# Performance work log

Hardware: AMD Instinct MI355X
Metric: run time of the kernel (lower is better)

The kernel has to match this reference:

```python
import jax, jax.numpy as jnp
import numpy as np

B, S, N, D = 2, 2048, 16, 64


def setup_inputs() -> dict:
    key = jax.random.key(0)
    kq, kk, kv = jax.random.split(key, 3)
    query = jax.random.normal(kq, (B, S, N, D), dtype=jnp.float32)
    key_t = jax.random.normal(kk, (B, S, N, D), dtype=jnp.float32)
    value = jax.random.normal(kv, (B, S, N, D), dtype=jnp.float32)
    mask = jnp.ones((B, 1, S, S), dtype=jnp.int32)
    return {"query": query, "key": key_t, "value": value, "mask": mask}


def reference(query, key, value, mask):
    d_k = query.shape[-1]
    # [b, n, q, k] attention scores
    scores = jnp.einsum('bqnd,bknd->bnqk', query, key) / jnp.sqrt(jnp.float32(d_k))
    scores = jnp.where(mask == 0, -jnp.inf, scores)
    # NOTE: faithful to the source, softmax is over dim=1 (the HEAD axis),
    # not the key axis. Dropout prob is 0.0 -> identity.
    attn_weights = jax.nn.softmax(scores, axis=1)
    out = jnp.einsum('bnqk,bknd->bnqd', attn_weights, value)
    return out
```

## Files before the change

### kernel.cpp

```cpp
#include <hip/hip_runtime.h>
#include <hip/hip_bf16.h>


#define B_ 2
#define S_ 2048
#define N_ 16
#define D_ 64
#define TQ 32
#define TK 32
#define NT 64

typedef __bf16 bf16x4 __attribute__((ext_vector_type(4)));
typedef __bf16 bf16x8 __attribute__((ext_vector_type(8)));
typedef float  f32x16 __attribute__((ext_vector_type(16)));
typedef unsigned int uint32x4 __attribute__((ext_vector_type(4)));

#define QSCALE 0.18033688011112042f

static __device__ __forceinline__ unsigned int cvt_pk_bf16(float a, float b) {
    unsigned int r;
    asm("v_cvt_pk_bf16_f32 %0, %1, %2" : "=v"(r) : "v"(a), "v"(b));
    return r;
}
static __device__ __forceinline__ void permlane_swap(unsigned int& a, unsigned int& b) {
    asm("v_permlane32_swap_b32 %0, %1" : "+v"(a), "+v"(b));
}

__global__ __launch_bounds__(256) void cvt_qk_pack_kernel(
    const float* __restrict__ Qf, const float* __restrict__ Kf,
    __bf16* __restrict__ QP, __bf16* __restrict__ KP)
{
    const int z = blockIdx.z;
    const float* src = (z < B_) ? Qf : Kf;
    __bf16*      dst = (z < B_) ? QP : KP;
    const float scale = (z < B_) ? QSCALE : 1.0f;
    const int b  = (z < B_) ? z : z - B_;
    const int n  = blockIdx.y;
    const int st = blockIdx.x;
    const int t  = threadIdx.x;
    const int ks   = t >> 6;
    const int lane = t & 63;
    const int lo   = lane & 31;
    const int hi   = lane >> 5;

    const float* p = &src[(((size_t)b * S_ + st * 32 + lo) * N_ + n) * D_ + ks * 16 + hi * 8];
    const float4 a0 = *(const float4*)p;
    const float4 a1 = *(const float4*)(p + 4);
    bf16x8 o;
    o[0] = (__bf16)(a0.x * scale); o[1] = (__bf16)(a0.y * scale);
    o[2] = (__bf16)(a0.z * scale); o[3] = (__bf16)(a0.w * scale);
    o[4] = (__bf16)(a1.x * scale); o[5] = (__bf16)(a1.y * scale);
    o[6] = (__bf16)(a1.z * scale); o[7] = (__bf16)(a1.w * scale);
    *(bf16x8*)&dst[(((size_t)b * N_ + n) * NT + st) * 2048 + (size_t)t * 8] = o;
}

__global__ __launch_bounds__(256) void cvt_v_pack_kernel(
    const float* __restrict__ V, __bf16* __restrict__ VP)
{
    __shared__ __bf16 tile[64][68];
    const int s0 = blockIdx.x * 64;
    const int n  = blockIdx.y;
    const int b  = blockIdx.z;
    const int t  = threadIdx.x;

    {
        const int d4 = (t & 15) * 4;
        const int sr = t >> 4;
        #pragma unroll
        for (int r = 0; r < 4; ++r) {
            const int s = sr + r * 16;
            const float4 v = *(const float4*)&V[(((size_t)b * S_ + s0 + s) * N_ + n) * D_ + d4];
            tile[s][d4 + 0] = (__bf16)v.x;
            tile[s][d4 + 1] = (__bf16)v.y;
            tile[s][d4 + 2] = (__bf16)v.z;
            tile[s][d4 + 3] = (__bf16)v.w;
        }
    }
    __syncthreads();
    {
        const int kstep = t >> 7;
        const int dt    = (t >> 6) & 1;
        const int lane  = t & 63;
        const int lo    = lane & 31;
        const int hi    = lane >> 5;
        #pragma unroll
        for (int kt_sub = 0; kt_sub < 2; ++kt_sub) {
            bf16x8 o;
            #pragma unroll
            for (int j = 0; j < 8; ++j)
                o[j] = tile[kt_sub * 32 + kstep * 16 + hi * 8 + j][dt * 32 + lo];
            const size_t kt = (size_t)(blockIdx.x * 2 + kt_sub);
            *(bf16x8*)&VP[(((size_t)b * N_ + n) * NT + kt) * 2048 + (size_t)t * 8] = o;
        }
    }
}

__global__ __launch_bounds__(256, 2) void pass1_z_kernel(
    const __bf16* __restrict__ QP, const __bf16* __restrict__ KP,
    const int* __restrict__ M, float* __restrict__ Zr)
{
    const int tid  = threadIdx.x;
    const int wv   = tid >> 6;
    const int lane = tid & 63;
    const int lo   = lane & 31;
    const int hi   = lane >> 5;

    const int ktA = (blockIdx.x * 4 + wv) * 2;
    const int qt0 = blockIdx.y * 2;
    const int b   = blockIdx.z;
    const int k0A = ktA * TK;
    const int q0  = qt0 * TQ;

    const __bf16* Qp = QP + ((size_t)b * N_ * NT + qt0) * 2048 + (size_t)lane * 8;
    const __bf16* Kp = KP + ((size_t)b * N_ * NT + ktA) * 2048 + (size_t)lane * 8;

    f32x16 zAA = {}, zAB = {}, zBA = {}, zBB = {};
    for (int h = 0; h < N_; ++h) {
        const __bf16* Qh = Qp + (size_t)h * NT * 2048;
        const __bf16* Kh = Kp + (size_t)h * NT * 2048;
        bf16x8 q0f[4], q1f[4], ka[4], kb[4];
        #pragma unroll
        for (int ks = 0; ks < 4; ++ks) {
            q0f[ks] = *(const bf16x8*)(Qh + ks * 512);
            q1f[ks] = *(const bf16x8*)(Qh + 2048 + ks * 512);
            ka[ks]  = *(const bf16x8*)(Kh + ks * 512);
            kb[ks]  = *(const bf16x8*)(Kh + 2048 + ks * 512);
        }
        f32x16 s;
        s = (f32x16){};
        #pragma unroll
        for (int ks = 0; ks < 4; ++ks) s = __builtin_amdgcn_mfma_f32_32x32x16_bf16(ka[ks], q0f[ks], s, 0, 0, 0);
        #pragma unroll
        for (int r = 0; r < 16; ++r) zAA[r] += __builtin_amdgcn_exp2f(s[r]);
        s = (f32x16){};
        #pragma unroll
        for (int ks = 0; ks < 4; ++ks) s = __builtin_amdgcn_mfma_f32_32x32x16_bf16(ka[ks], q1f[ks], s, 0, 0, 0);
        #pragma unroll
        for (int r = 0; r < 16; ++r) zAB[r] += __builtin_amdgcn_exp2f(s[r]);
        s = (f32x16){};
        #pragma unroll
        for (int ks = 0; ks < 4; ++ks) s = __builtin_amdgcn_mfma_f32_32x32x16_bf16(kb[ks], q0f[ks], s, 0, 0, 0);
        #pragma unroll
        for (int r = 0; r < 16; ++r) zBA[r] += __builtin_amdgcn_exp2f(s[r]);
        s = (f32x16){};
        #pragma unroll
        for (int ks = 0; ks < 4; ++ks) s = __builtin_amdgcn_mfma_f32_32x32x16_bf16(kb[ks], q1f[ks], s, 0, 0, 0);
        #pragma unroll
        for (int r = 0; r < 16; ++r) zBB[r] += __builtin_amdgcn_exp2f(s[r]);
    }

    const size_t mb = (size_t)b * S_ * S_;
    int ok = 1;
    #pragma unroll
    for (int r = 0; r < 16; ++r) {
        const int4 mm = *(const int4*)&M[mb + (size_t)(q0 + 4 * r + (lane >> 4)) * S_
                                         + k0A + (lane & 15) * 4];
        ok &= (mm.x != 0) & (mm.y != 0) & (mm.z != 0) & (mm.w != 0);
    }

    float vAA[16], vAB[16], vBA[16], vBB[16];
    #pragma unroll
    for (int r = 0; r < 16; ++r) {
        vAA[r] = __builtin_amdgcn_rcpf(zAA[r]);
        vAB[r] = __builtin_amdgcn_rcpf(zAB[r]);
        vBA[r] = __builtin_amdgcn_rcpf(zBA[r]);
        vBB[r] = __builtin_amdgcn_rcpf(zBB[r]);
    }

    if (!__all(ok)) {
        #pragma unroll
        for (int r = 0; r < 16; ++r) {
            const int kap = (r & 3) + 8 * (r >> 2) + 4 * hi;
            const size_t rowA = mb + (size_t)(q0 + lo) * S_;
            const size_t rowB = mb + (size_t)(q0 + 32 + lo) * S_;
            if (M[rowA + k0A + kap] == 0)      vAA[r] = __builtin_nanf("");
            if (M[rowB + k0A + kap] == 0)      vAB[r] = __builtin_nanf("");
            if (M[rowA + k0A + 32 + kap] == 0) vBA[r] = __builtin_nanf("");
            if (M[rowB + k0A + 32 + kap] == 0) vBB[r] = __builtin_nanf("");
        }
    }

    auto store_tile = [&](const float (&v)[16], int kt_, int qt_) {
        float* Zt = Zr + (((size_t)b * NT + kt_) * NT + qt_) * 1024 + (size_t)lane * 4;
        #pragma unroll
        for (int c = 0; c < 4; ++c)
            *(float4*)(Zt + c * 256) = make_float4(v[4*c], v[4*c+1], v[4*c+2], v[4*c+3]);
    };
    store_tile(vAA, ktA,     qt0);
    store_tile(vAB, ktA,     qt0 + 1);
    store_tile(vBA, ktA + 1, qt0);
    store_tile(vBB, ktA + 1, qt0 + 1);
}

__global__ __launch_bounds__(256, 4) void pass2_av_kernel(
    const __bf16* __restrict__ QP, const __bf16* __restrict__ KP,
    const __bf16* __restrict__ VP, const float* __restrict__ Zr,
    float* __restrict__ O)
{
    __shared__ __align__(16) float obuf[4][16 * D_];

    const int tid  = threadIdx.x;
    const int wv   = tid >> 6;
    const int lane = tid & 63;
    const int lo   = lane & 31;
    const int hi   = lane >> 5;

    const int qt = blockIdx.x;
    const int n  = blockIdx.y;
    const int b  = blockIdx.z;
    const int q0 = qt * TQ;

    const __bf16* Qh = QP + (((size_t)b * N_ + n) * NT + qt) * 2048 + (size_t)lane * 8;
    const __bf16* Kh = KP + (((size_t)b * N_ + n) * NT) * 2048 + (size_t)lane * 8;
    const __bf16* Vh = VP + (((size_t)b * N_ + n) * NT) * 2048 + (size_t)lane * 8;
    const float*  Zb = Zr + (size_t)b * NT * NT * 1024 + (size_t)lane * 4;

    bf16x8 qf[4];
    #pragma unroll
    for (int ks = 0; ks < 4; ++ks)
        qf[ks] = *(const bf16x8*)(Qh + ks * 512);

    f32x16 o0 = {};
    f32x16 o1 = {};

    #pragma unroll 2
    for (int t = 0; t < 16; ++t) {
        const int kt = wv * 16 + t;
        const __bf16* Kt = Kh + (size_t)kt * 2048;
        const __bf16* Vt = Vh + (size_t)kt * 2048;
        const float*  Zt = Zb + ((size_t)kt * NT + qt) * 1024;

        float4 z0 = *(const float4*)(Zt);
        float4 z1 = *(const float4*)(Zt + 256);
        float4 z2 = *(const float4*)(Zt + 512);
        float4 z3 = *(const float4*)(Zt + 768);
        float zr[16] = { z0.x, z0.y, z0.z, z0.w,  z1.x, z1.y, z1.z, z1.w,
                         z2.x, z2.y, z2.z, z2.w,  z3.x, z3.y, z3.z, z3.w };

        bf16x8 kf[4];
        #pragma unroll
        for (int ks = 0; ks < 4; ++ks) kf[ks] = *(const bf16x8*)(Kt + ks * 512);
        bf16x8 vf[2][2];
        #pragma unroll
        for (int kstep = 0; kstep < 2; ++kstep)
            #pragma unroll
            for (int dt = 0; dt < 2; ++dt)
                vf[kstep][dt] = *(const bf16x8*)(Vt + (kstep * 2 + dt) * 512);

        f32x16 s = {};
        #pragma unroll
        for (int ks = 0; ks < 4; ++ks)
            s = __builtin_amdgcn_mfma_f32_32x32x16_bf16(kf[ks], qf[ks], s, 0, 0, 0);

        float w[16];
        #pragma unroll
        for (int r = 0; r < 16; ++r) w[r] = __builtin_amdgcn_exp2f(s[r]) * zr[r];

        #pragma unroll
        for (int kstep = 0; kstep < 2; ++kstep) {
            const int e = kstep * 8;
            unsigned int d0 = cvt_pk_bf16(w[e + 0], w[e + 1]);
            unsigned int d1 = cvt_pk_bf16(w[e + 2], w[e + 3]);
            unsigned int d2 = cvt_pk_bf16(w[e + 4], w[e + 5]);
            unsigned int d3 = cvt_pk_bf16(w[e + 6], w[e + 7]);
            permlane_swap(d0, d2);
            permlane_swap(d1, d3);
            uint32x4 u; u[0] = d0; u[1] = d1; u[2] = d2; u[3] = d3;
            const bf16x8 pa = __builtin_bit_cast(bf16x8, u);
            o0 = __builtin_amdgcn_mfma_f32_32x32x16_bf16(pa, vf[kstep][0], o0, 0, 0, 0);
            o1 = __builtin_amdgcn_mfma_f32_32x32x16_bf16(pa, vf[kstep][1], o1, 0, 0, 0);
        }
    }

    #pragma unroll
    for (int half = 0; half < 2; ++half) {
        if (half) __syncthreads();
        #pragma unroll
        for (int r8 = 0; r8 < 8; ++r8) {
            const int r  = half * 8 + r8;
            const int lr = (r8 & 3) + 8 * (r8 >> 2) + 4 * hi;
            obuf[wv][lr * D_ + lo]      = o0[r];
            obuf[wv][lr * D_ + 32 + lo] = o1[r];
        }
        __syncthreads();
        const int e0 = tid * 4;
        float a0 = 0.f, a1 = 0.f, a2 = 0.f, a3 = 0.f;
        #pragma unroll
        for (int w = 0; w < 4; ++w) {
            const float4 x = *(const float4*)&obuf[w][e0];
            a0 += x.x; a1 += x.y; a2 += x.z; a3 += x.w;
        }
        const int q = half * 16 + (e0 >> 6);
        const int d = e0 & 63;
        *(float4*)&O[(((size_t)b * N_ + n) * S_ + q0 + q) * (size_t)D_ + d]
            = make_float4(a0, a1, a2, a3);
    }
}

__global__ __launch_bounds__(1024) void sdpa_headsm_kernel(
    const float* __restrict__ Q, const float* __restrict__ K,
    const float* __restrict__ V, const int* __restrict__ M,
    float* __restrict__ O)
{
    __shared__ __align__(16) __bf16 pbuf[N_][TQ][40];

    const int tid  = threadIdx.x;
    const int n    = tid >> 6;
    const int lane = tid & 63;
    const int lo   = lane & 31;
    const int hi   = lane >> 5;

    const int q0 = blockIdx.x * TQ;
    const int b  = blockIdx.y;
    const int kz = blockIdx.z;
    const int FITERS = S_ / TK / 4;

    bf16x8 qf[4];
    {
        const float* qrow = Q + (((size_t)b * S_ + (size_t)(q0 + lo)) * N_ + n) * D_;
        #pragma unroll
        for (int ks = 0; ks < 4; ++ks) {
            const float* p = qrow + ks * 16 + hi * 8;
            float4 a0 = *(const float4*)(p);
            float4 a1 = *(const float4*)(p + 4);
            bf16x8 f;
            f[0] = (__bf16)a0.x; f[1] = (__bf16)a0.y;
            f[2] = (__bf16)a0.z; f[3] = (__bf16)a0.w;
            f[4] = (__bf16)a1.x; f[5] = (__bf16)a1.y;
            f[6] = (__bf16)a1.z; f[7] = (__bf16)a1.w;
            qf[ks] = f;
        }
    }

    f32x16 o0 = {};
    f32x16 o1 = {};

    for (int it = 0; it < FITERS; ++it) {
        const int k0 = (kz * FITERS + it) * TK;

        f32x16 s = {};
        #pragma unroll
        for (int ks = 0; ks < 4; ++ks) {
            const float* krow = K + (((size_t)b * S_ + (size_t)(k0 + lo)) * N_ + n) * D_
                                  + ks * 16 + hi * 8;
            float4 a0 = *(const float4*)(krow);
            float4 a1 = *(const float4*)(krow + 4);
            bf16x8 f;
            f[0] = (__bf16)a0.x; f[1] = (__bf16)a0.y;
            f[2] = (__bf16)a0.z; f[3] = (__bf16)a0.w;
            f[4] = (__bf16)a1.x; f[5] = (__bf16)a1.y;
            f[6] = (__bf16)a1.z; f[7] = (__bf16)a1.w;
            s = __builtin_amdgcn_mfma_f32_32x32x16_bf16(qf[ks], f, s, 0, 0, 0);
        }

        bf16x8 vf[2][2];
        #pragma unroll
        for (int kstep = 0; kstep < 2; ++kstep) {
            #pragma unroll
            for (int dt = 0; dt < 2; ++dt) {
                bf16x8 f;
                #pragma unroll
                for (int j = 0; j < 8; ++j) {
                    const int key = k0 + kstep * 16 + hi * 8 + j;
                    f[j] = (__bf16)V[(((size_t)b * S_ + key) * N_ + n) * D_ + dt * 32 + lo];
                }
                vf[kstep][dt] = f;
            }
        }

        #pragma unroll
        for (int r = 0; r < 16; ++r) {
            const int row = (r & 3) + 8 * (r >> 2) + 4 * hi;
            pbuf[n][row][lo] = (__bf16)__builtin_amdgcn_exp2f(s[r] * QSCALE);
        }

        __syncthreads();

        {
            const int tq = tid >> 5;
            const int tk = tid & 31;
            const int m = M[(size_t)b * S_ * S_ + (size_t)(q0 + tq) * S_ + (k0 + tk)];
            float pv[16];
            float sum = 0.f;
            #pragma unroll
            for (int j = 0; j < 16; ++j) { pv[j] = (float)pbuf[j][tq][tk]; sum += pv[j]; }
            const float rd = m ? (1.0f / sum) : __builtin_nanf("");
            #pragma unroll
            for (int j = 0; j < 16; ++j) pbuf[j][tq][tk] = (__bf16)(pv[j] * rd);
        }

        __syncthreads();

        #pragma unroll
        for (int kstep = 0; kstep < 2; ++kstep) {
            bf16x8 wf = *(const bf16x8*)&pbuf[n][lo][kstep * 16 + hi * 8];
            o0 = __builtin_amdgcn_mfma_f32_32x32x16_bf16(wf, vf[kstep][0], o0, 0, 0, 0);
            o1 = __builtin_amdgcn_mfma_f32_32x32x16_bf16(wf, vf[kstep][1], o1, 0, 0, 0);
        }

        __syncthreads();
    }

    #pragma unroll
    for (int r = 0; r < 16; ++r) {
        const int row = (r & 3) + 8 * (r >> 2) + 4 * hi;
        const size_t base = (((size_t)b * N_ + n) * S_ + (q0 + row)) * (size_t)D_;
        atomicAdd(&O[base + lo],      o0[r]);
        atomicAdd(&O[base + 32 + lo], o1[r]);
    }
}

extern "C" void kernel_launch(void* const* d_in, const int* in_sizes, int n_in,
                              void* d_out, int out_size, void* d_ws, size_t ws_size,
                              hipStream_t stream) {
    const float* Q = (const float*)d_in[0];
    const float* K = (const float*)d_in[1];
    const float* V = (const float*)d_in[2];
    const int*   M = (const int*)d_in[3];
    float* O = (float*)d_out;

    const size_t per  = (size_t)B_ * N_ * NT * 2048;
    const size_t zcnt = (size_t)B_ * NT * NT * 1024;
    const size_t need = 3 * per * sizeof(__bf16) + zcnt * sizeof(float);

    if (ws_size >= need) {
        __bf16* QP = (__bf16*)d_ws;
        __bf16* KP = QP + per;
        __bf16* VP = KP + per;
        float*  Zr = (float*)(VP + per);
        cvt_qk_pack_kernel<<<dim3(NT, N_, B_ * 2), dim3(256), 0, stream>>>(Q, K, QP, KP);
        cvt_v_pack_kernel<<<dim3(S_ / 64, N_, B_), dim3(256), 0, stream>>>(V, VP);
        pass1_z_kernel<<<dim3(NT / 8, NT / 2, B_), dim3(256), 0, stream>>>(QP, KP, M, Zr);
        pass2_av_kernel<<<dim3(NT, N_, B_), dim3(256), 0, stream>>>(QP, KP, VP, Zr, O);
    } else {
        hipMemsetAsync(d_out, 0, (size_t)out_size * sizeof(float), stream);
        sdpa_headsm_kernel<<<dim3(S_ / TQ, B_, 4), dim3(1024), 0, stream>>>(Q, K, V, M, O);
    }
}
```

Before: 212.7 us.

## Merge pack kernels, unroll pass1 head loop, double-buffer K loads in pass2

```diff
diff --git a/kernel.cpp b/kernel.cpp
--- a/kernel.cpp
+++ b/kernel.cpp
@@ -26,71 +26,70 @@
     asm("v_permlane32_swap_b32 %0, %1" : "+v"(a), "+v"(b));
 }
 
-__global__ __launch_bounds__(256) void cvt_qk_pack_kernel(
+__global__ __launch_bounds__(256) void cvt_pack_kernel(
     const float* __restrict__ Qf, const float* __restrict__ Kf,
-    __bf16* __restrict__ QP, __bf16* __restrict__ KP)
-{
-    const int z = blockIdx.z;
-    const float* src = (z < B_) ? Qf : Kf;
-    __bf16*      dst = (z < B_) ? QP : KP;
-    const float scale = (z < B_) ? QSCALE : 1.0f;
-    const int b  = (z < B_) ? z : z - B_;
-    const int n  = blockIdx.y;
-    const int st = blockIdx.x;
-    const int t  = threadIdx.x;
-    const int ks   = t >> 6;
-    const int lane = t & 63;
-    const int lo   = lane & 31;
-    const int hi   = lane >> 5;
-
-    const float* p = &src[(((size_t)b * S_ + st * 32 + lo) * N_ + n) * D_ + ks * 16 + hi * 8];
-    const float4 a0 = *(const float4*)p;
-    const float4 a1 = *(const float4*)(p + 4);
-    bf16x8 o;
-    o[0] = (__bf16)(a0.x * scale); o[1] = (__bf16)(a0.y * scale);
-    o[2] = (__bf16)(a0.z * scale); o[3] = (__bf16)(a0.w * scale);
-    o[4] = (__bf16)(a1.x * scale); o[5] = (__bf16)(a1.y * scale);
-    o[6] = (__bf16)(a1.z * scale); o[7] = (__bf16)(a1.w * scale);
-    *(bf16x8*)&dst[(((size_t)b * N_ + n) * NT + st) * 2048 + (size_t)t * 8] = o;
-}
-
-__global__ __launch_bounds__(256) void cvt_v_pack_kernel(
-    const float* __restrict__ V, __bf16* __restrict__ VP)
+    const float* __restrict__ Vf,
+    __bf16* __restrict__ QP, __bf16* __restrict__ KP, __bf16* __restrict__ VP)
 {
     __shared__ __bf16 tile[64][68];
-    const int s0 = blockIdx.x * 64;
-    const int n  = blockIdx.y;
-    const int b  = blockIdx.z;
-    const int t  = threadIdx.x;
-
-    {
-        const int d4 = (t & 15) * 4;
-        const int sr = t >> 4;
-        #pragma unroll
-        for (int r = 0; r < 4; ++r) {
-            const int s = sr + r * 16;
-            const float4 v = *(const float4*)&V[(((size_t)b * S_ + s0 + s) * N_ + n) * D_ + d4];
-            tile[s][d4 + 0] = (__bf16)v.x;
-            tile[s][d4 + 1] = (__bf16)v.y;
-            tile[s][d4 + 2] = (__bf16)v.z;
-            tile[s][d4 + 3] = (__bf16)v.w;
-        }
-    }
-    __syncthreads();
-    {
-        const int kstep = t >> 7;
-        const int dt    = (t >> 6) & 1;
-        const int lane  = t & 63;
-        const int lo    = lane & 31;
-        const int hi    = lane >> 5;
-        #pragma unroll
-        for (int kt_sub = 0; kt_sub < 2; ++kt_sub) {
-            bf16x8 o;
-            #pragma unroll
-            for (int j = 0; j < 8; ++j)
-                o[j] = tile[kt_sub * 32 + kstep * 16 + hi * 8 + j][dt * 32 + lo];
-            const size_t kt = (size_t)(blockIdx.x * 2 + kt_sub);
-            *(bf16x8*)&VP[(((size_t)b * N_ + n) * NT + kt) * 2048 + (size_t)t * 8] = o;
+    const int z = blockIdx.z;
+    const int t = threadIdx.x;
+
+    if (z < 2 * B_) {
+        const float* src = (z < B_) ? Qf : Kf;
+        __bf16*      dst = (z < B_) ? QP : KP;
+        const float scale = (z < B_) ? QSCALE : 1.0f;
+        const int b  = (z < B_) ? z : z - B_;
+        const int n  = blockIdx.y;
+        const int st = blockIdx.x;
+        const int ks   = t >> 6;
+        const int lane = t & 63;
+        const int lo   = lane & 31;
+        const int hi   = lane >> 5;
+
+        const float* p = &src[(((size_t)b * S_ + st * 32 + lo) * N_ + n) * D_ + ks * 16 + hi * 8];
+        const float4 a0 = *(const float4*)p;
+        const float4 a1 = *(const float4*)(p + 4);
+        bf16x8 o;
+        o[0] = (__bf16)(a0.x * scale); o[1] = (__bf16)(a0.y * scale);
+        o[2] = (__bf16)(a0.z * scale); o[3] = (__bf16)(a0.w * scale);
+        o[4] = (__bf16)(a1.x * scale); o[5] = (__bf16)(a1.y * scale);
+        o[6] = (__bf16)(a1.z * scale); o[7] = (__bf16)(a1.w * scale);
+        *(bf16x8*)&dst[(((size_t)b * N_ + n) * NT + st) * 2048 + (size_t)t * 8] = o;
+    } else {
+        if (blockIdx.x >= S_ / 64) return;
+        const int b  = z - 2 * B_;
+        const int s0 = blockIdx.x * 64;
+        const int n  = blockIdx.y;
+        {
+            const int d4 = (t & 15) * 4;
+            const int sr = t >> 4;
+            #pragma unroll
+            for (int r = 0; r < 4; ++r) {
+                const int s = sr + r * 16;
+                const float4 v = *(const float4*)&Vf[(((size_t)b * S_ + s0 + s) * N_ + n) * D_ + d4];
+                tile[s][d4 + 0] = (__bf16)v.x;
+                tile[s][d4 + 1] = (__bf16)v.y;
+                tile[s][d4 + 2] = (__bf16)v.z;
+                tile[s][d4 + 3] = (__bf16)v.w;
+            }
+        }
+        __syncthreads();
+        {
+            const int kstep = t >> 7;
+            const int dt    = (t >> 6) & 1;
+            const int lane  = t & 63;
+            const int lo    = lane & 31;
+            const int hi    = lane >> 5;
+            #pragma unroll
+            for (int kt_sub = 0; kt_sub < 2; ++kt_sub) {
+                bf16x8 o;
+                #pragma unroll
+                for (int j = 0; j < 8; ++j)
+                    o[j] = tile[kt_sub * 32 + kstep * 16 + hi * 8 + j][dt * 32 + lo];
+                const size_t kt = (size_t)(blockIdx.x * 2 + kt_sub);
+                *(bf16x8*)&VP[(((size_t)b * N_ + n) * NT + kt) * 2048 + (size_t)t * 8] = o;
+            }
         }
     }
 }
@@ -115,6 +114,7 @@
     const __bf16* Kp = KP + ((size_t)b * N_ * NT + ktA) * 2048 + (size_t)lane * 8;
 
     f32x16 zAA = {}, zAB = {}, zBA = {}, zBB = {};
+    #pragma unroll 2
     for (int h = 0; h < N_; ++h) {
         const __bf16* Qh = Qp + (size_t)h * NT * 2048;
         const __bf16* Kh = Kp + (size_t)h * NT * 2048;
@@ -192,7 +192,7 @@
     store_tile(vBB, ktA + 1, qt0 + 1);
 }
 
-__global__ __launch_bounds__(256, 4) void pass2_av_kernel(
+__global__ __launch_bounds__(256, 3) void pass2_av_kernel(
     const __bf16* __restrict__ QP, const __bf16* __restrict__ KP,
     const __bf16* __restrict__ VP, const float* __restrict__ Zr,
     float* __restrict__ O)
@@ -211,9 +211,10 @@
     const int q0 = qt * TQ;
 
     const __bf16* Qh = QP + (((size_t)b * N_ + n) * NT + qt) * 2048 + (size_t)lane * 8;
-    const __bf16* Kh = KP + (((size_t)b * N_ + n) * NT) * 2048 + (size_t)lane * 8;
-    const __bf16* Vh = VP + (((size_t)b * N_ + n) * NT) * 2048 + (size_t)lane * 8;
-    const float*  Zb = Zr + (size_t)b * NT * NT * 1024 + (size_t)lane * 4;
+    const __bf16* Kw = KP + (((size_t)b * N_ + n) * NT + wv * 16) * 2048 + (size_t)lane * 8;
+    const __bf16* Vw = VP + (((size_t)b * N_ + n) * NT + wv * 16) * 2048 + (size_t)lane * 8;
+    const float*  Zw = Zr + ((size_t)b * NT * NT + (size_t)(wv * 16) * NT + qt) * 1024
+                          + (size_t)lane * 4;
 
     bf16x8 qf[4];
     #pragma unroll
@@ -223,12 +224,15 @@
     f32x16 o0 = {};
     f32x16 o1 = {};
 
-    #pragma unroll 2
+    bf16x8 kf[2][4];
+    #pragma unroll
+    for (int ks = 0; ks < 4; ++ks)
+        kf[0][ks] = *(const bf16x8*)(Kw + ks * 512);
+
+    #pragma unroll
     for (int t = 0; t < 16; ++t) {
-        const int kt = wv * 16 + t;
-        const __bf16* Kt = Kh + (size_t)kt * 2048;
-        const __bf16* Vt = Vh + (size_t)kt * 2048;
-        const float*  Zt = Zb + ((size_t)kt * NT + qt) * 1024;
+        const __bf16* Vt = Vw + (size_t)t * 2048;
+        const float*  Zt = Zw + (size_t)t * (NT * 1024);
 
         float4 z0 = *(const float4*)(Zt);
         float4 z1 = *(const float4*)(Zt + 256);
@@ -237,9 +241,6 @@
         float zr[16] = { z0.x, z0.y, z0.z, z0.w,  z1.x, z1.y, z1.z, z1.w,
                          z2.x, z2.y, z2.z, z2.w,  z3.x, z3.y, z3.z, z3.w };
 
-        bf16x8 kf[4];
-        #pragma unroll
-        for (int ks = 0; ks < 4; ++ks) kf[ks] = *(const bf16x8*)(Kt + ks * 512);
         bf16x8 vf[2][2];
         #pragma unroll
         for (int kstep = 0; kstep < 2; ++kstep)
@@ -247,10 +248,17 @@
             for (int dt = 0; dt < 2; ++dt)
                 vf[kstep][dt] = *(const bf16x8*)(Vt + (kstep * 2 + dt) * 512);
 
+        if (t + 1 < 16) {
+            const __bf16* Kn = Kw + (size_t)(t + 1) * 2048;
+            #pragma unroll
+            for (int ks = 0; ks < 4; ++ks)
+                kf[(t + 1) & 1][ks] = *(const bf16x8*)(Kn + ks * 512);
+        }
+
         f32x16 s = {};
         #pragma unroll
         for (int ks = 0; ks < 4; ++ks)
-            s = __builtin_amdgcn_mfma_f32_32x32x16_bf16(kf[ks], qf[ks], s, 0, 0, 0);
+            s = __builtin_amdgcn_mfma_f32_32x32x16_bf16(kf[t & 1][ks], qf[ks], s, 0, 0, 0);
 
         float w[16];
         #pragma unroll
@@ -428,8 +436,7 @@
         __bf16* KP = QP + per;
         __bf16* VP = KP + per;
         float*  Zr = (float*)(VP + per);
-        cvt_qk_pack_kernel<<<dim3(NT, N_, B_ * 2), dim3(256), 0, stream>>>(Q, K, QP, KP);
-        cvt_v_pack_kernel<<<dim3(S_ / 64, N_, B_), dim3(256), 0, stream>>>(V, VP);
+        cvt_pack_kernel<<<dim3(NT, N_, 3 * B_), dim3(256), 0, stream>>>(Q, K, V, QP, KP, VP);
         pass1_z_kernel<<<dim3(NT / 8, NT / 2, B_), dim3(256), 0, stream>>>(QP, KP, M, Zr);
         pass2_av_kernel<<<dim3(NT, N_, B_), dim3(256), 0, stream>>>(QP, KP, VP, Zr, O);
     } else {
```

Result: no change. 209.5 us (-1.5%).
